# Optimization experiments

Measured on AMD Instinct MI355X. Metric: run time of the kernel, lower is better.

## Reference

```python
import jax, jax.numpy as jnp
import numpy as np

L = 12        # depth
DIM = 768     # model dim
HEADS = 12
DHEAD = 64
INNER = HEADS * DHEAD   # 768
MLP = 3072
P = 16        # patch size
IMG = 384
C = 3
B = 16
NCLS = 1000
NPATCH = (IMG // P) ** 2   # 576
N = NPATCH + 1             # 577 (cls token)
PATCH_DIM = C * P * P      # 768
SCALE = DIM ** (-0.5)      # NOTE: original scales by dim, not dim_head


def setup_inputs() -> dict:
    key = jax.random.key(0)
    ks = jax.random.split(key, 21)
    rn = lambda k, shape, s=0.02: jax.random.normal(k, shape, dtype=jnp.float32) * s
    return {
        "img": jax.random.normal(ks[0], (B, C, IMG, IMG), dtype=jnp.float32),
        "patch_w": rn(ks[1], (PATCH_DIM, DIM)),
        "patch_b": rn(ks[2], (DIM,)),
        "pos_emb": rn(ks[3], (1, N, DIM), 1.0),
        "cls_tok": rn(ks[4], (1, 1, DIM), 1.0),
        "ln1_w": jnp.ones((L, DIM), jnp.float32),
        "ln1_b": jnp.zeros((L, DIM), jnp.float32),
        "qkv_w": rn(ks[5], (L, DIM, 3 * INNER)),
        "out_w": rn(ks[6], (L, INNER, DIM)),
        "out_b": rn(ks[7], (L, DIM)),
        "ln2_w": jnp.ones((L, DIM), jnp.float32),
        "ln2_b": jnp.zeros((L, DIM), jnp.float32),
        "ff1_w": rn(ks[8], (L, DIM, MLP)),
        "ff1_b": rn(ks[9], (L, MLP)),
        "ff2_w": rn(ks[10], (L, MLP, DIM)),
        "ff2_b": rn(ks[11], (L, DIM)),
        "head_ln_w": jnp.ones((DIM,), jnp.float32),
        "head_ln_b": jnp.zeros((DIM,), jnp.float32),
        "head_w": rn(ks[12], (DIM, NCLS)),
        "head_b": rn(ks[13], (NCLS,)),
    }


def layer_norm(x, w, b, eps=1e-5):
    mu = jnp.mean(x, axis=-1, keepdims=True)
    var = jnp.mean(jnp.square(x - mu), axis=-1, keepdims=True)
    return (x - mu) * jax.lax.rsqrt(var + eps) * w + b


def _vit_forward(img, patch_w, patch_b, pos_emb, cls_tok,
                 ln1_w, ln1_b, qkv_w, out_w, out_b,
                 ln2_w, ln2_b, ff1_w, ff1_b, ff2_w, ff2_b,
                 head_ln_w, head_ln_b, head_w, head_b):
    b = img.shape[0]
    g = IMG // P
    # rearrange 'b c (h p1) (w p2) -> b (h w) (p1 p2 c)'
    x = img.reshape(b, C, g, P, g, P).transpose(0, 2, 4, 3, 5, 1).reshape(b, NPATCH, PATCH_DIM)
    x = x @ patch_w + patch_b                           # [b, 576, dim]
    cls = jnp.broadcast_to(cls_tok, (b, 1, DIM))
    x = jnp.concatenate([cls, x], axis=1) + pos_emb[:, :N]   # [b, 577, dim]

    def block(x, p):
        l1w, l1b, qkvw, ow, ob, l2w, l2b, f1w, f1b, f2w, f2b = p
        # attention (pre-norm, residual inside Attention.forward)
        h = layer_norm(x, l1w, l1b)
        qkv = h @ qkvw                                  # [b, n, 3*inner]
        q, k, v = jnp.split(qkv, 3, axis=-1)
        to_heads = lambda t: t.reshape(b, N, HEADS, DHEAD).transpose(0, 2, 1, 3)
        q, k, v = to_heads(q), to_heads(k), to_heads(v)  # [b, h, n, d]
        dots = jnp.einsum('bhid,bhjd->bhij', q, k) * SCALE
        attn = jax.nn.softmax(dots, axis=-1)
        o = jnp.einsum('bhij,bhjd->bhid', attn, v)
        o = o.transpose(0, 2, 1, 3).reshape(b, N, INNER)
        x = x + (o @ ow + ob)
        # feedforward (pre-norm, residual)
        h2 = layer_norm(x, l2w, l2b)
        h2 = jax.nn.gelu(h2 @ f1w + f1b, approximate=False)
        x = x + (h2 @ f2w + f2b)
        return x, None

    x, _ = jax.lax.scan(block, x,
                        (ln1_w, ln1_b, qkv_w, out_w, out_b,
                         ln2_w, ln2_b, ff1_w, ff1_b, ff2_w, ff2_b))
    cls_out = x[:, 0]                                   # [b, dim]
    return layer_norm(cls_out, head_ln_w, head_ln_b) @ head_w + head_b


def reference(img, patch_w, patch_b, pos_emb, cls_tok,
              ln1_w, ln1_b, qkv_w, out_w, out_b,
              ln2_w, ln2_b, ff1_w, ff1_b, ff2_w, ff2_b,
              head_ln_w, head_ln_b, head_w, head_b):
    return _vit_forward(img, patch_w, patch_b, pos_emb, cls_tok,
                        ln1_w, ln1_b, qkv_w, out_w, out_b,
                        ln2_w, ln2_b, ff1_w, ff1_b, ff2_w, ff2_b,
                        head_ln_w, head_ln_b, head_w, head_b)
```

## Files before the change

kernel.cpp:

```cpp
#include <hip/hip_runtime.h>
#include <cstdint>


typedef __attribute__((ext_vector_type(8))) short bf16x8;
typedef __attribute__((ext_vector_type(4))) float f32x4;

#define NTOK 577

__device__ __forceinline__ ushort f2bf(float f) {
  union { float f; unsigned int u; } x; x.f = f;
  unsigned int r = x.u + 0x7fffu + ((x.u >> 16) & 1u);
  return (ushort)(r >> 16);
}
__device__ __forceinline__ float bf2f(ushort u) {
  union { unsigned int u; float f; } x; x.u = ((unsigned int)u) << 16;
  return x.f;
}

__device__ __forceinline__ void gload_lds16(const ushort* g, ushort* l) {
  __builtin_amdgcn_global_load_lds(
      (const __attribute__((address_space(1))) unsigned int*)g,
      (__attribute__((address_space(3))) unsigned int*)l, 16, 0, 0);
}

#define VMCNT0 asm volatile("s_waitcnt vmcnt(0)" ::: "memory")
#define LGKM0  asm volatile("s_waitcnt lgkmcnt(0)" ::: "memory")
#define SCHED0 __builtin_amdgcn_sched_barrier(0)
#define BARRIER __builtin_amdgcn_s_barrier()

__device__ __forceinline__ int gsw(int row) {
  return (row & 7) + 2 * ((row >> 4) & 3);
}

__device__ __forceinline__ void transpose_tile(const float* __restrict__ W,
                                               ushort* __restrict__ Wt,
                                               int K, int N, int kb, int nb,
                                               int tx, int ty, float t[32][33]) {
#pragma unroll
  for (int i = 0; i < 32; i += 8)
    t[ty + i][tx] = W[(size_t)(kb + ty + i) * N + (nb + tx)];
  __syncthreads();
#pragma unroll
  for (int i = 0; i < 32; i += 8)
    Wt[(size_t)(nb + ty + i) * K + (kb + tx)] = f2bf(t[tx][ty + i]);
}

__global__ __launch_bounds__(256) void convt_kernel(const float* __restrict__ W,
                                                    ushort* __restrict__ Wt,
                                                    int K, int N) {
  __shared__ float t[32][33];
  transpose_tile(W, Wt, K, N, blockIdx.x * 32, blockIdx.y * 32,
                 threadIdx.x & 31, threadIdx.x >> 5, t);
}

__global__ __launch_bounds__(256) void wconv_kernel(
    const float* __restrict__ qkv_w, const float* __restrict__ out_w,
    const float* __restrict__ ff1_w, const float* __restrict__ ff2_w,
    ushort* __restrict__ wq, ushort* __restrict__ wo,
    ushort* __restrict__ w1, ushort* __restrict__ w2) {
  __shared__ float t[32][33];
  const int tx = threadIdx.x & 31, ty = threadIdx.x >> 5;
  int bx = blockIdx.x;
  if (bx < 1728) {
    transpose_tile(qkv_w, wq, 768, 2304, (bx % 24) * 32, (bx / 24) * 32, tx, ty, t);
  } else if (bx < 2304) {
    bx -= 1728;
    transpose_tile(out_w, wo, 768, 768, (bx % 24) * 32, (bx / 24) * 32, tx, ty, t);
  } else if (bx < 4608) {
    bx -= 2304;
    transpose_tile(ff1_w, w1, 768, 3072, (bx % 24) * 32, (bx / 24) * 32, tx, ty, t);
  } else {
    bx -= 4608;
    transpose_tile(ff2_w, w2, 3072, 768, (bx % 96) * 32, (bx / 96) * 32, tx, ty, t);
  }
}

__global__ __launch_bounds__(256) void im2col_kernel(const float* __restrict__ img,
                                                     ushort* __restrict__ Ap) {
  const int idx = blockIdx.x * 256 + threadIdx.x;
  const int j = idx % 768;
  const int m = idx / 768;
  const int c = j % 3;
  const int q = j / 3;
  const int px = q & 15, py = q >> 4;
  const int b = m / 576, p = m % 576;
  const int gy = p / 24, gx = p % 24;
  const float v = img[((size_t)(b * 3 + c) * 384 + (gy * 16 + py)) * 384 + (gx * 16 + px)];
  Ap[idx] = f2bf(v);
}

__global__ void clspos_kernel(const float* __restrict__ cls_tok,
                              const float* __restrict__ pos,
                              ushort* __restrict__ x) {
  const int i = blockIdx.x * 256 + threadIdx.x;
  const int b = i / 768, d = i % 768;
  x[(size_t)b * NTOK * 768 + d] = f2bf(cls_tok[d] + pos[d]);
}

__global__ __launch_bounds__(256) void ln_kernel(const ushort* __restrict__ x,
                                                 const float* __restrict__ w,
                                                 const float* __restrict__ bb,
                                                 ushort* __restrict__ out) {
  const int wave = threadIdx.x >> 6, lane = threadIdx.x & 63;
  const int row = blockIdx.x * 4 + wave;
  const ushort* xr = x + (size_t)row * 768;
  float vals[12];
#pragma unroll
  for (int ch = 0; ch < 3; ++ch) {
    const ushort4 u = *reinterpret_cast<const ushort4*>(xr + ch * 256 + lane * 4);
    vals[ch * 4 + 0] = bf2f(u.x);
    vals[ch * 4 + 1] = bf2f(u.y);
    vals[ch * 4 + 2] = bf2f(u.z);
    vals[ch * 4 + 3] = bf2f(u.w);
  }
  float s = 0.f;
#pragma unroll
  for (int i = 0; i < 12; ++i) s += vals[i];
#pragma unroll
  for (int o = 32; o; o >>= 1) s += __shfl_xor(s, o);
  const float mu = s * (1.0f / 768.0f);
  float q = 0.f;
#pragma unroll
  for (int i = 0; i < 12; ++i) { const float d = vals[i] - mu; q += d * d; }
#pragma unroll
  for (int o = 32; o; o >>= 1) q += __shfl_xor(q, o);
  const float rstd = rsqrtf(q * (1.0f / 768.0f) + 1e-5f);
  const float4* w4 = reinterpret_cast<const float4*>(w);
  const float4* b4 = reinterpret_cast<const float4*>(bb);
  ushort* orow = out + (size_t)row * 768;
#pragma unroll
  for (int ch = 0; ch < 3; ++ch) {
    const float4 wv = w4[lane + ch * 64];
    const float4 bv = b4[lane + ch * 64];
    ushort4 u;
    u.x = f2bf((vals[ch * 4 + 0] - mu) * rstd * wv.x + bv.x);
    u.y = f2bf((vals[ch * 4 + 1] - mu) * rstd * wv.y + bv.y);
    u.z = f2bf((vals[ch * 4 + 2] - mu) * rstd * wv.z + bv.z);
    u.w = f2bf((vals[ch * 4 + 3] - mu) * rstd * wv.w + bv.w);
    *reinterpret_cast<ushort4*>(orow + ch * 256 + lane * 4) = u;
  }
}

constexpr int EPI_BF16 = 0;
constexpr int EPI_GELU_BF16 = 1;
constexpr int EPI_RES = 2;
constexpr int EPI_PATCH = 3;

template <int EPI>
__global__ __launch_bounds__(512, 2) void gemm8_kernel(
    const ushort* __restrict__ A, const ushort* __restrict__ Bt,
    const float* __restrict__ bias, void* __restrict__ Cptr,
    int M, int N, int K, int nt) {
  __shared__ ushort lds[2][2][16384];

  const int nwg = gridDim.x;
  const int orig = blockIdx.x;
  const int q8 = nwg >> 3, r8 = nwg & 7, xcd = orig & 7, sidx = orig >> 3;
  const int wg = (xcd < r8 ? xcd * (q8 + 1) : r8 * (q8 + 1) + (xcd - r8) * q8) + sidx;
  const int tileM = (wg / nt) * 256;
  const int tileN = (wg % nt) * 256;

  const int tid = threadIdx.x;
  const int wave = tid >> 6, lane = tid & 63;
  const int wm = wave >> 2, wn = wave & 3;
  const int lr = lane & 15, lg = lane >> 4;

  f32x4 acc[8][4];
#pragma unroll
  for (int i = 0; i < 8; ++i)
#pragma unroll
    for (int j = 0; j < 4; ++j) acc[i][j] = (f32x4){0.f, 0.f, 0.f, 0.f};

  int rsA[2][2], rsB[2][2];
  const ushort* pA[2][2];
  const ushort* pB[2][2];
#pragma unroll
  for (int h = 0; h < 2; ++h)
#pragma unroll
    for (int g = 0; g < 2; ++g) {
      const int c = wave * 2 + g;
      {
        const int rowst = h * 64 + ((c >> 3) << 7) + ((c & 7) << 3);
        rsA[h][g] = rowst;
        const int row = rowst + (lane >> 3);
        const int lgr = ((lane & 7) - gsw(row)) & 7;
        pA[h][g] = A + (size_t)(tileM + row) * K + lgr * 8;
      }
      {
        const int rowst = h * 32 + ((c >> 2) << 6) + ((c & 3) << 3);
        rsB[h][g] = rowst;
        const int row = rowst + (lane >> 3);
        const int lgr = ((lane & 7) - gsw(row)) & 7;
        pB[h][g] = Bt + (size_t)(tileN + row) * K + lgr * 8;
      }
    }

#define STAGE_A(h, buf, k1)                                   \
  gload_lds16(pA[h][0] + (k1), &lds[buf][0][rsA[h][0] * 64]); \
  gload_lds16(pA[h][1] + (k1), &lds[buf][0][rsA[h][1] * 64]);
#define STAGE_B(h, buf, k1)                                   \
  gload_lds16(pB[h][0] + (k1), &lds[buf][1][rsB[h][0] * 64]); \
  gload_lds16(pB[h][1] + (k1), &lds[buf][1][rsB[h][1] * 64]);

  bf16x8 areg[8], breg[8];
#define LDA8(h, buf)                                                          \
  {                                                                           \
    const ushort* base = &lds[buf][0][0];                                     \
    _Pragma("unroll") for (int mf = 0; mf < 4; ++mf) {                        \
      const int row = wm * 128 + (h) * 64 + mf * 16 + lr;                     \
      _Pragma("unroll") for (int ks = 0; ks < 2; ++ks) {                      \
        const int pg = (ks * 4 + lg + (lr & 7) + 2 * mf) & 7;                 \
        areg[mf * 2 + ks] =                                                   \
            *reinterpret_cast<const bf16x8*>(&base[row * 64 + pg * 8]);       \
      }                                                                       \
    }                                                                         \
  }
#define LDB8(buf)                                                             \
  {                                                                           \
    const ushort* base = &lds[buf][1][0];                                     \
    _Pragma("unroll") for (int q = 0; q < 2; ++q)                             \
        _Pragma("unroll") for (int nf = 0; nf < 2; ++nf) {                    \
      const int row = wn * 64 + q * 32 + nf * 16 + lr;                        \
      _Pragma("unroll") for (int ks = 0; ks < 2; ++ks) {                      \
        const int pg = (ks * 4 + lg + (lr & 7) + 2 * ((q * 2 + nf) & 3)) & 7; \
        breg[q * 4 + nf * 2 + ks] =                                           \
            *reinterpret_cast<const bf16x8*>(&base[row * 64 + pg * 8]);       \
      }                                                                       \
    }                                                                         \
  }
#define MFMA32(h)                                                           \
  __builtin_amdgcn_s_setprio(1);                                            \
  _Pragma("unroll") for (int q = 0; q < 2; ++q)                             \
      _Pragma("unroll") for (int mf = 0; mf < 4; ++mf)                      \
          _Pragma("unroll") for (int nf = 0; nf < 2; ++nf)                  \
              _Pragma("unroll") for (int ks = 0; ks < 2; ++ks)              \
                  acc[(h)*4 + mf][q * 2 + nf] =                             \
                      __builtin_amdgcn_mfma_f32_16x16x32_bf16(              \
                          areg[mf * 2 + ks], breg[q * 4 + nf * 2 + ks],     \
                          acc[(h)*4 + mf][q * 2 + nf], 0, 0, 0);            \
  __builtin_amdgcn_s_setprio(0);

  STAGE_A(0, 0, 0);
  STAGE_B(0, 0, 0);
  STAGE_B(1, 0, 0);
  STAGE_A(1, 0, 0);

  const int NT = K >> 6;
  for (int t = 0; t < NT - 1; ++t) {
    const int cb = t & 1, nb = (t + 1) & 1;
    const int k1 = (t + 1) * 64;
    VMCNT0; SCHED0;
    BARRIER;
    STAGE_A(0, nb, k1);
    STAGE_B(0, nb, k1);
    STAGE_B(1, nb, k1);
    STAGE_A(1, nb, k1);
    LDA8(0, cb);
    LDB8(cb);
    LGKM0; SCHED0;
    MFMA32(0);
    LDA8(1, cb);
    LGKM0; SCHED0;
    MFMA32(1);
  }

  {
    const int cb = (NT - 1) & 1;
    VMCNT0; SCHED0;
    BARRIER;
    LDA8(0, cb);
    LDB8(cb);
    LGKM0; SCHED0;
    MFMA32(0);
    LDA8(1, cb);
    LGKM0; SCHED0;
    MFMA32(1);
  }

#pragma unroll
  for (int am = 0; am < 8; ++am) {
#pragma unroll
    for (int r = 0; r < 4; ++r) {
      const int row = tileM + wm * 128 + (am >> 2) * 64 + (am & 3) * 16 + lg * 4 + r;
      if (row >= M) continue;
#pragma unroll
      for (int an = 0; an < 4; ++an) {
        const int col = tileN + wn * 64 + (an >> 1) * 32 + (an & 1) * 16 + lr;
        float v = acc[am][an][r];
        if constexpr (EPI == EPI_BF16) {
          reinterpret_cast<ushort*>(Cptr)[(size_t)row * N + col] = f2bf(v);
        } else {
          v += bias[col];
          v = 0.5f * v * (1.0f + erff(v * 0.70710678118654752440f));
          reinterpret_cast<ushort*>(Cptr)[(size_t)row * N + col] = f2bf(v);
        }
      }
    }
  }
#undef STAGE_A
#undef STAGE_B
#undef LDA8
#undef LDB8
#undef MFMA32
}

template <int EPI>
__global__ __launch_bounds__(256) void gemmP_kernel(
    const ushort* __restrict__ A, const ushort* __restrict__ Bt,
    const float* __restrict__ bias, const void* __restrict__ extra,
    void* __restrict__ Cptr, int M, int N, int K, int mt) {
  __shared__ ushort ldsA[2][128 * 64];
  __shared__ ushort ldsB[2][128 * 64];

  const int nwg = gridDim.x;
  const int orig = blockIdx.x;
  const int q8 = nwg >> 3, r8 = nwg & 7, xcd = orig & 7, sidx = orig >> 3;
  const int wg = (xcd < r8 ? xcd * (q8 + 1) : r8 * (q8 + 1) + (xcd - r8) * q8) + sidx;
  const int tileM = (wg % mt) * 128;
  const int tileN = (wg / mt) * 128;

  const int tid = threadIdx.x;
  const int wave = tid >> 6, lane = tid & 63;
  const int wm = wave >> 1, wn = wave & 1;
  const int lr = lane & 15, lg = lane >> 4;

  f32x4 acc[4][4];
#pragma unroll
  for (int m = 0; m < 4; ++m)
#pragma unroll
    for (int n = 0; n < 4; ++n) acc[m][n] = (f32x4){0.f, 0.f, 0.f, 0.f};

  const ushort* pA[4];
  const ushort* pB[4];
  int dst[4];
#pragma unroll
  for (int i = 0; i < 4; ++i) {
    const int c = wave * 4 + i;
    const int rowst = c * 8;
    dst[i] = rowst * 64;
    const int row = rowst + (lane >> 3);
    const int lgr = ((lane & 7) - gsw(row)) & 7;
    pA[i] = A + (size_t)(tileM + row) * K + lgr * 8;
    pB[i] = Bt + (size_t)(tileN + row) * K + lgr * 8;
  }

#define PSTAGE(buf, kk)                              \
  _Pragma("unroll") for (int i = 0; i < 4; ++i)      \
      gload_lds16(pA[i] + (kk), &ldsA[buf][dst[i]]); \
  _Pragma("unroll") for (int i = 0; i < 4; ++i)      \
      gload_lds16(pB[i] + (kk), &ldsB[buf][dst[i]]);

  PSTAGE(0, 0);

  const int NT = K >> 6;
  int cb = 0;
  for (int t = 0; t < NT; ++t) {
    VMCNT0; SCHED0;
    BARRIER;
    if (t + 1 < NT) { PSTAGE(cb ^ 1, (t + 1) * 64); }
    bf16x8 a[8], b[8];
#pragma unroll
    for (int mf = 0; mf < 4; ++mf) {
      const int row = wm * 64 + mf * 16 + lr;
#pragma unroll
      for (int ks = 0; ks < 2; ++ks) {
        const int pg = (ks * 4 + lg + (lr & 7) + 2 * mf) & 7;
        a[mf * 2 + ks] = *reinterpret_cast<const bf16x8*>(&ldsA[cb][row * 64 + pg * 8]);
      }
    }
#pragma unroll
    for (int nf = 0; nf < 4; ++nf) {
      const int row = wn * 64 + nf * 16 + lr;
#pragma unroll
      for (int ks = 0; ks < 2; ++ks) {
        const int pg = (ks * 4 + lg + (lr & 7) + 2 * nf) & 7;
        b[nf * 2 + ks] = *reinterpret_cast<const bf16x8*>(&ldsB[cb][row * 64 + pg * 8]);
      }
    }
    LGKM0; SCHED0;
    __builtin_amdgcn_s_setprio(1);
#pragma unroll
    for (int mf = 0; mf < 4; ++mf)
#pragma unroll
      for (int nf = 0; nf < 4; ++nf)
#pragma unroll
        for (int ks = 0; ks < 2; ++ks)
          acc[mf][nf] = __builtin_amdgcn_mfma_f32_16x16x32_bf16(
              a[mf * 2 + ks], b[nf * 2 + ks], acc[mf][nf], 0, 0, 0);
    __builtin_amdgcn_s_setprio(0);
    cb ^= 1;
  }

#pragma unroll
  for (int mf = 0; mf < 4; ++mf) {
#pragma unroll
    for (int r = 0; r < 4; ++r) {
      const int row = tileM + wm * 64 + mf * 16 + lg * 4 + r;
      if (row >= M) continue;
#pragma unroll
      for (int nf = 0; nf < 4; ++nf) {
        const int col = tileN + wn * 64 + nf * 16 + lr;
        float v = acc[mf][nf][r];
        if constexpr (EPI == EPI_BF16) {
          reinterpret_cast<ushort*>(Cptr)[(size_t)row * N + col] = f2bf(v);
        } else if constexpr (EPI == EPI_GELU_BF16) {
          v += bias[col];
          v = 0.5f * v * (1.0f + erff(v * 0.70710678118654752440f));
          reinterpret_cast<ushort*>(Cptr)[(size_t)row * N + col] = f2bf(v);
        } else if constexpr (EPI == EPI_RES) {
          v += bias[col] +
               bf2f(reinterpret_cast<const ushort*>(extra)[(size_t)row * N + col]);
          reinterpret_cast<ushort*>(Cptr)[(size_t)row * N + col] = f2bf(v);
        } else {
          const int bb = row / 576;
          const int p = row - bb * 576;
          v += bias[col] +
               reinterpret_cast<const float*>(extra)[(size_t)(p + 1) * 768 + col];
          reinterpret_cast<ushort*>(Cptr)[(size_t)(row + bb + 1) * 768 + col] = f2bf(v);
        }
      }
    }
  }
#undef PSTAGE
}

__global__ __launch_bounds__(256) void attn_kernel(const ushort* __restrict__ qkv,
                                                   ushort* __restrict__ o) {
  __shared__ ushort sK[64 * 64];
  __shared__ ushort sVt[64 * 64];
  __shared__ ushort sP[4][16 * 72];
  const int bh = blockIdx.x;
  const int b = bh / 12, hh = bh % 12;
  const int q0 = blockIdx.y * 64;
  const int tid = threadIdx.x;
  const int wave = tid >> 6, lane = tid & 63;
  const int lr = lane & 15;
  const int lg = lane >> 4;
  const ushort* base = qkv + (size_t)b * NTOK * 2304 + hh * 64;
  const float SC = 0.03608439182435161f;

  bf16x8 qf[2];
  {
    const int qrow = q0 + wave * 16 + lr;
    if (qrow < NTOK) {
      const ushort* qp = base + (size_t)qrow * 2304 + lg * 8;
      qf[0] = *reinterpret_cast<const bf16x8*>(qp);
      qf[1] = *reinterpret_cast<const bf16x8*>(qp + 32);
    } else {
      qf[0] = (bf16x8){0, 0, 0, 0, 0, 0, 0, 0};
      qf[1] = qf[0];
    }
  }

  float mst[4], lst[4];
  f32x4 oacc[4];
#pragma unroll
  for (int i = 0; i < 4; ++i) {
    mst[i] = -1e30f; lst[i] = 0.f;
    oacc[i] = (f32x4){0.f, 0.f, 0.f, 0.f};
  }

  const int skey = tid >> 2;
  const int sc4 = tid & 3;
  const int gswk = gsw(skey);

  for (int t0 = 0; t0 < NTOK; t0 += 64) {
    __syncthreads();
    {
      const int gk = t0 + skey;
      int4 k0v, k1v, v0v, v1v;
      if (gk < NTOK) {
        const int4* kp = reinterpret_cast<const int4*>(base + (size_t)gk * 2304 + 768 + sc4 * 16);
        k0v = kp[0]; k1v = kp[1];
        const int4* vp = reinterpret_cast<const int4*>(base + (size_t)gk * 2304 + 1536 + sc4 * 16);
        v0v = vp[0]; v1v = vp[1];
      } else {
        int4 z; z.x = z.y = z.z = z.w = 0;
        k0v = k1v = v0v = v1v = z;
      }
      *reinterpret_cast<int4*>(&sK[skey * 64 + (((2 * sc4 + 0) + gswk) & 7) * 8]) = k0v;
      *reinterpret_cast<int4*>(&sK[skey * 64 + (((2 * sc4 + 1) + gswk) & 7) * 8]) = k1v;
      const ushort* vs = reinterpret_cast<const ushort*>(&v0v);
      const ushort* vs2 = reinterpret_cast<const ushort*>(&v1v);
#pragma unroll
      for (int i = 0; i < 8; ++i) {
        const int d0 = sc4 * 16 + i;
        const int pg0 = ((skey >> 3) + gsw(d0)) & 7;
        sVt[d0 * 64 + pg0 * 8 + (skey & 7)] = vs[i];
        const int d1 = sc4 * 16 + 8 + i;
        const int pg1 = ((skey >> 3) + gsw(d1)) & 7;
        sVt[d1 * 64 + pg1 * 8 + (skey & 7)] = vs2[i];
      }
    }
    __syncthreads();

    f32x4 sacc[4];
#pragma unroll
    for (int n = 0; n < 4; ++n) sacc[n] = (f32x4){0.f, 0.f, 0.f, 0.f};
#pragma unroll
    for (int n = 0; n < 4; ++n) {
      const int row = n * 16 + lr;
      const int rot = (lr & 7) + 2 * n;
      const bf16x8 kf0 = *reinterpret_cast<const bf16x8*>(&sK[row * 64 + ((lg + rot) & 7) * 8]);
      const bf16x8 kf1 = *reinterpret_cast<const bf16x8*>(&sK[row * 64 + ((4 + lg + rot) & 7) * 8]);
      sacc[n] = __builtin_amdgcn_mfma_f32_16x16x32_bf16(qf[0], kf0, sacc[n], 0, 0, 0);
      sacc[n] = __builtin_amdgcn_mfma_f32_16x16x32_bf16(qf[1], kf1, sacc[n], 0, 0, 0);
    }

    float s[4][4], pm[4];
#pragma unroll
    for (int reg = 0; reg < 4; ++reg) pm[reg] = -1e30f;
#pragma unroll
    for (int n = 0; n < 4; ++n)
#pragma unroll
      for (int reg = 0; reg < 4; ++reg) {
        float v = sacc[n][reg] * SC;
        if (t0 + n * 16 + lr >= NTOK) v = -1e30f;
        s[n][reg] = v;
        pm[reg] = fmaxf(pm[reg], v);
      }
#pragma unroll
    for (int off = 1; off < 16; off <<= 1)
#pragma unroll
      for (int reg = 0; reg < 4; ++reg) pm[reg] = fmaxf(pm[reg], __shfl_xor(pm[reg], off));

    float al[4], rs[4];
#pragma unroll
    for (int reg = 0; reg < 4; ++reg) {
      const float mn = fmaxf(mst[reg], pm[reg]);
      al[reg] = __expf(mst[reg] - mn);
      mst[reg] = mn;
      rs[reg] = 0.f;
    }
#pragma unroll
    for (int n = 0; n < 4; ++n)
#pragma unroll
      for (int reg = 0; reg < 4; ++reg) {
        s[n][reg] = __expf(s[n][reg] - mst[reg]);
        rs[reg] += s[n][reg];
      }
#pragma unroll
    for (int off = 1; off < 16; off <<= 1)
#pragma unroll
      for (int reg = 0; reg < 4; ++reg) rs[reg] += __shfl_xor(rs[reg], off);
#pragma unroll
    for (int reg = 0; reg < 4; ++reg) {
      lst[reg] = lst[reg] * al[reg] + rs[reg];
#pragma unroll
      for (int n = 0; n < 4; ++n) oacc[n][reg] *= al[reg];
    }

#pragma unroll
    for (int n = 0; n < 4; ++n)
#pragma unroll
      for (int reg = 0; reg < 4; ++reg)
        sP[wave][(lg * 4 + reg) * 72 + n * 16 + lr] = f2bf(s[n][reg]);

    const bf16x8 pf0 = *reinterpret_cast<const bf16x8*>(&sP[wave][lr * 72 + lg * 8]);
    const bf16x8 pf1 = *reinterpret_cast<const bf16x8*>(&sP[wave][lr * 72 + 32 + lg * 8]);
#pragma unroll
    for (int n = 0; n < 4; ++n) {
      const int row = n * 16 + lr;
      const int rot = (lr & 7) + 2 * n;
      const bf16x8 vf0 = *reinterpret_cast<const bf16x8*>(&sVt[row * 64 + ((lg + rot) & 7) * 8]);
      const bf16x8 vf1 = *reinterpret_cast<const bf16x8*>(&sVt[row * 64 + ((4 + lg + rot) & 7) * 8]);
      oacc[n] = __builtin_amdgcn_mfma_f32_16x16x32_bf16(pf0, vf0, oacc[n], 0, 0, 0);
      oacc[n] = __builtin_amdgcn_mfma_f32_16x16x32_bf16(pf1, vf1, oacc[n], 0, 0, 0);
    }
  }

#pragma unroll
  for (int reg = 0; reg < 4; ++reg) {
    const int q = q0 + wave * 16 + lg * 4 + reg;
    if (q >= NTOK) continue;
    const float inv = 1.0f / lst[reg];
    ushort* op = o + (size_t)(b * NTOK + q) * 768 + hh * 64;
#pragma unroll
    for (int n = 0; n < 4; ++n) op[n * 16 + lr] = f2bf(oacc[n][reg] * inv);
  }
}

__global__ __launch_bounds__(256) void head_kernel(const ushort* __restrict__ x,
                                                   const float* __restrict__ lw,
                                                   const float* __restrict__ lb,
                                                   const float* __restrict__ hw,
                                                   const float* __restrict__ hb,
                                                   float* __restrict__ out) {
  __shared__ float srow[768];
  __shared__ float sred[8];
  __shared__ float spart[4][64];
  const int b = blockIdx.x, ct = blockIdx.y, tid = threadIdx.x;
  const ushort* xr = x + (size_t)b * NTOK * 768;
  for (int i = tid; i < 768; i += 256) srow[i] = bf2f(xr[i]);
  __syncthreads();
  float part = srow[tid] + srow[tid + 256] + srow[tid + 512];
#pragma unroll
  for (int off = 32; off; off >>= 1) part += __shfl_xor(part, off);
  if ((tid & 63) == 0) sred[tid >> 6] = part;
  __syncthreads();
  const float mu = (sred[0] + sred[1] + sred[2] + sred[3]) * (1.0f / 768.0f);
  const float d0 = srow[tid] - mu, d1 = srow[tid + 256] - mu, d2 = srow[tid + 512] - mu;
  float vp = d0 * d0 + d1 * d1 + d2 * d2;
#pragma unroll
  for (int off = 32; off; off >>= 1) vp += __shfl_xor(vp, off);
  if ((tid & 63) == 0) sred[4 + (tid >> 6)] = vp;
  __syncthreads();
  const float rstd = rsqrtf((sred[4] + sred[5] + sred[6] + sred[7]) * (1.0f / 768.0f) + 1e-5f);
  for (int i = tid; i < 768; i += 256) srow[i] = (srow[i] - mu) * rstd * lw[i] + lb[i];
  __syncthreads();
  const int cl = tid & 63, kq = tid >> 6;
  const int c = ct * 64 + cl;
  float a = 0.f;
  if (c < 1000) {
    const int k0 = kq * 192;
#pragma unroll 8
    for (int k = k0; k < k0 + 192; ++k) a += srow[k] * hw[(size_t)k * 1000 + c];
  }
  spart[kq][cl] = a;
  __syncthreads();
  if (tid < 64) {
    const int c2 = ct * 64 + tid;
    if (c2 < 1000)
      out[b * 1000 + c2] =
          spart[0][tid] + spart[1][tid] + spart[2][tid] + spart[3][tid] + hb[c2];
  }
}

extern "C" void kernel_launch(void* const* d_in, const int* in_sizes, int n_in,
                              void* d_out, int out_size, void* d_ws, size_t ws_size,
                              hipStream_t stream) {
  const float* img     = (const float*)d_in[0];
  const float* patch_w = (const float*)d_in[1];
  const float* patch_b = (const float*)d_in[2];
  const float* pos_emb = (const float*)d_in[3];
  const float* cls_tok = (const float*)d_in[4];
  const float* ln1_w   = (const float*)d_in[5];
  const float* ln1_b   = (const float*)d_in[6];
  const float* qkv_w   = (const float*)d_in[7];
  const float* out_w   = (const float*)d_in[8];
  const float* out_b   = (const float*)d_in[9];
  const float* ln2_w   = (const float*)d_in[10];
  const float* ln2_b   = (const float*)d_in[11];
  const float* ff1_w   = (const float*)d_in[12];
  const float* ff1_b   = (const float*)d_in[13];
  const float* ff2_w   = (const float*)d_in[14];
  const float* ff2_b   = (const float*)d_in[15];
  const float* hln_w   = (const float*)d_in[16];
  const float* hln_b   = (const float*)d_in[17];
  const float* head_w  = (const float*)d_in[18];
  const float* head_b  = (const float*)d_in[19];
  float* outp = (float*)d_out;

  char* wsp = (char*)d_ws;
  auto alloc = [&](size_t bytes) {
    char* p = wsp;
    wsp += (bytes + 255) & ~(size_t)255;
    return p;
  };
  ushort* x    = (ushort*)alloc((size_t)9232 * 768 * 2);
  ushort* h    = (ushort*)alloc((size_t)9232 * 768 * 2);
  ushort* qkvb = (ushort*)alloc((size_t)9232 * 2304 * 2);
  ushort* mlp  = (ushort*)alloc((size_t)9232 * 3072 * 2);
  ushort* wq   = (ushort*)alloc((size_t)768 * 2304 * 2);
  ushort* wo   = (ushort*)alloc((size_t)768 * 768 * 2);
  ushort* w1   = (ushort*)alloc((size_t)768 * 3072 * 2);
  ushort* w2   = (ushort*)alloc((size_t)3072 * 768 * 2);
  ushort* apatch = mlp;
  ushort* wpatch = wq;

  convt_kernel<<<dim3(24, 24), 256, 0, stream>>>(patch_w, wpatch, 768, 768);
  im2col_kernel<<<27648, 256, 0, stream>>>(img, apatch);
  gemmP_kernel<EPI_PATCH><<<72 * 6, 256, 0, stream>>>(
      apatch, wpatch, patch_b, pos_emb, x, 9216, 768, 768, 72);
  clspos_kernel<<<48, 256, 0, stream>>>(cls_tok, pos_emb, x);

  for (int l = 0; l < 12; ++l) {
    wconv_kernel<<<6912, 256, 0, stream>>>(
        qkv_w + (size_t)l * 768 * 2304, out_w + (size_t)l * 768 * 768,
        ff1_w + (size_t)l * 768 * 3072, ff2_w + (size_t)l * 3072 * 768,
        wq, wo, w1, w2);
    ln_kernel<<<2308, 256, 0, stream>>>(x, ln1_w + l * 768, ln1_b + l * 768, h);
    gemm8_kernel<EPI_BF16><<<37 * 9, 512, 0, stream>>>(
        h, wq, nullptr, qkvb, 9232, 2304, 768, 9);
    attn_kernel<<<dim3(192, 10), 256, 0, stream>>>(qkvb, h);
    gemmP_kernel<EPI_RES><<<73 * 6, 256, 0, stream>>>(
        h, wo, out_b + l * 768, x, x, 9232, 768, 768, 73);
    ln_kernel<<<2308, 256, 0, stream>>>(x, ln2_w + l * 768, ln2_b + l * 768, h);
    gemm8_kernel<EPI_GELU_BF16><<<37 * 12, 512, 0, stream>>>(
        h, w1, ff1_b + l * 3072, mlp, 9232, 3072, 768, 12);
    gemmP_kernel<EPI_RES><<<73 * 6, 256, 0, stream>>>(
        mlp, w2, ff2_b + l * 768, x, x, 9232, 768, 3072, 73);
  }

  head_kernel<<<dim3(16, 16), 256, 0, stream>>>(x, hln_w, hln_b, head_w, head_b, outp);
}
```

Before: 4.014 ms.

## Add single-buffered 128x128 GEMM kernel for FF1 with GELU epilogue

Adds a new 256-thread GEMM kernel with 128x128 tiles and a single LDS buffer, loading through direct global-to-LDS copies and computing with 16x16x32 bf16 MFMAs. It replaces the 512-thread gemm8 kernel for the FF1 projection with GELU. The smaller tiles give many more workgroups (73*24), so more blocks can be resident per CU and the tail is smaller. The cost is no double buffering inside a block, so overlapping loads with compute relies on other resident blocks.

```diff
diff --git a/kernel.cpp b/kernel.cpp
--- a/kernel.cpp
+++ b/kernel.cpp
@@ -302,6 +302,113 @@
 #undef LDA8
 #undef LDB8
 #undef MFMA32
+}
+
+template <int EPI>
+__global__ __launch_bounds__(256) void gemmS_kernel(
+    const ushort* __restrict__ A, const ushort* __restrict__ Bt,
+    const float* __restrict__ bias, void* __restrict__ Cptr,
+    int M, int N, int K, int nt) {
+  __shared__ ushort ldsA[128 * 64];
+  __shared__ ushort ldsB[128 * 64];
+
+  const int nwg = gridDim.x;
+  const int orig = blockIdx.x;
+  const int q8 = nwg >> 3, r8 = nwg & 7, xcd = orig & 7, sidx = orig >> 3;
+  const int wg = (xcd < r8 ? xcd * (q8 + 1) : r8 * (q8 + 1) + (xcd - r8) * q8) + sidx;
+  const int tileM = (wg / nt) * 128;
+  const int tileN = (wg % nt) * 128;
+
+  const int tid = threadIdx.x;
+  const int wave = tid >> 6, lane = tid & 63;
+  const int wm = wave >> 1, wn = wave & 1;
+  const int lr = lane & 15, lg = lane >> 4;
+
+  f32x4 acc[4][4];
+#pragma unroll
+  for (int m = 0; m < 4; ++m)
+#pragma unroll
+    for (int n = 0; n < 4; ++n) acc[m][n] = (f32x4){0.f, 0.f, 0.f, 0.f};
+
+  const ushort* pA[4];
+  const ushort* pB[4];
+  int dst[4];
+#pragma unroll
+  for (int i = 0; i < 4; ++i) {
+    const int c = wave * 4 + i;
+    const int rowst = c * 8;
+    dst[i] = rowst * 64;
+    const int row = rowst + (lane >> 3);
+    const int lgr = ((lane & 7) - gsw(row)) & 7;
+    pA[i] = A + (size_t)(tileM + row) * K + lgr * 8;
+    pB[i] = Bt + (size_t)(tileN + row) * K + lgr * 8;
+  }
+
+#define SSTAGE(kk)                                     \
+  _Pragma("unroll") for (int i = 0; i < 4; ++i)        \
+      gload_lds16(pA[i] + (kk), &ldsA[dst[i]]);        \
+  _Pragma("unroll") for (int i = 0; i < 4; ++i)        \
+      gload_lds16(pB[i] + (kk), &ldsB[dst[i]]);
+
+  const int NT = K >> 6;
+  for (int t = 0; t < NT; ++t) {
+    if (t) BARRIER;
+    SSTAGE(t * 64);
+    VMCNT0; SCHED0;
+    BARRIER;
+    bf16x8 a[8], b[8];
+#pragma unroll
+    for (int mf = 0; mf < 4; ++mf) {
+      const int row = wm * 64 + mf * 16 + lr;
+#pragma unroll
+      for (int ks = 0; ks < 2; ++ks) {
+        const int pg = (ks * 4 + lg + (lr & 7) + 2 * mf) & 7;
+        a[mf * 2 + ks] = *reinterpret_cast<const bf16x8*>(&ldsA[row * 64 + pg * 8]);
+      }
+    }
+#pragma unroll
+    for (int nf = 0; nf < 4; ++nf) {
+      const int row = wn * 64 + nf * 16 + lr;
+#pragma unroll
+      for (int ks = 0; ks < 2; ++ks) {
+        const int pg = (ks * 4 + lg + (lr & 7) + 2 * nf) & 7;
+        b[nf * 2 + ks] = *reinterpret_cast<const bf16x8*>(&ldsB[row * 64 + pg * 8]);
+      }
+    }
+    LGKM0; SCHED0;
+    __builtin_amdgcn_s_setprio(1);
+#pragma unroll
+    for (int mf = 0; mf < 4; ++mf)
+#pragma unroll
+      for (int nf = 0; nf < 4; ++nf)
+#pragma unroll
+        for (int ks = 0; ks < 2; ++ks)
+          acc[mf][nf] = __builtin_amdgcn_mfma_f32_16x16x32_bf16(
+              a[mf * 2 + ks], b[nf * 2 + ks], acc[mf][nf], 0, 0, 0);
+    __builtin_amdgcn_s_setprio(0);
+  }
+
+#pragma unroll
+  for (int mf = 0; mf < 4; ++mf) {
+#pragma unroll
+    for (int r = 0; r < 4; ++r) {
+      const int row = tileM + wm * 64 + mf * 16 + lg * 4 + r;
+      if (row >= M) continue;
+#pragma unroll
+      for (int nf = 0; nf < 4; ++nf) {
+        const int col = tileN + wn * 64 + nf * 16 + lr;
+        float v = acc[mf][nf][r];
+        if constexpr (EPI == EPI_BF16) {
+          reinterpret_cast<ushort*>(Cptr)[(size_t)row * N + col] = f2bf(v);
+        } else {
+          v += bias[col];
+          v = 0.5f * v * (1.0f + erff(v * 0.70710678118654752440f));
+          reinterpret_cast<ushort*>(Cptr)[(size_t)row * N + col] = f2bf(v);
+        }
+      }
+    }
+  }
+#undef SSTAGE
 }
 
 template <int EPI>
@@ -686,8 +793,8 @@
     gemmP_kernel<EPI_RES><<<73 * 6, 256, 0, stream>>>(
         h, wo, out_b + l * 768, x, x, 9232, 768, 768, 73);
     ln_kernel<<<2308, 256, 0, stream>>>(x, ln2_w + l * 768, ln2_b + l * 768, h);
-    gemm8_kernel<EPI_GELU_BF16><<<37 * 12, 512, 0, stream>>>(
-        h, w1, ff1_b + l * 3072, mlp, 9232, 3072, 768, 12);
+    gemmS_kernel<EPI_GELU_BF16><<<73 * 24, 256, 0, stream>>>(
+        h, w1, ff1_b + l * 3072, mlp, 9232, 3072, 768, 24);
     gemmP_kernel<EPI_RES><<<73 * 6, 256, 0, stream>>>(
         mlp, w2, ff2_b + l * 768, x, x, 9232, 768, 3072, 73);
   }
```

Result: no change. 4.089 ms (+1.9%).
